# Kernel tuning notes

Hardware: AMD Instinct MI355X
Metric: run time of the kernel (lower is better)

The kernel has to match this reference:

```python
import jax, jax.numpy as jnp
import numpy as np

N_HEAD = 16
EPS = 1e-6


def setup_inputs() -> dict:
    key = jax.random.key(0)
    k1, k2, k3 = jax.random.split(key, 3)
    B, T, C = 2, 2048, 1024
    x = jax.random.normal(k1, (B, T, C), dtype=jnp.float32)
    w_attn = jax.random.normal(k2, (C, 3 * C), dtype=jnp.float32) * 0.02
    w_proj = jax.random.normal(k3, (C, C), dtype=jnp.float32) * 0.02
    return {"x": x, "w_attn": w_attn, "w_proj": w_proj}


def _linear_attention(q, k, v):
    """q,k,v: (T,B,H,D) with q,k already feature-mapped (elu+1).
    Causal linear attention via a D x D running-state recurrence (same math
    as cumsum of k-v outer products, computed without the O(T*D^2) tensor)."""
    B, H, D = q.shape[1], q.shape[2], q.shape[3]

    def step(carry, qkv_t):
        S, z = carry                      # S:(B,H,D,D), z:(B,H,D)
        qt, kt, vt = qkv_t                # each (B,H,D)
        S = S + kt[..., :, None] * vt[..., None, :]
        z = z + kt
        num = jnp.einsum('bhi,bhij->bhj', qt, S)
        den = jnp.sum(qt * z, axis=-1, keepdims=True)
        return (S, z), num / (den + EPS)

    S0 = jnp.zeros((B, H, D, D), q.dtype)
    z0 = jnp.zeros((B, H, D), q.dtype)
    _, y = jax.lax.scan(step, (S0, z0), (q, k, v))
    return y                              # (T,B,H,D)


def reference(x, w_attn, w_proj):
    B, T, C = x.shape
    H = N_HEAD
    D = C // H
    qkv = x @ w_attn                      # (B,T,3C)
    q, k, v = jnp.split(qkv, 3, axis=-1)

    def to_tbhd(a):                       # (B,T,C) -> (T,B,H,D)
        return a.reshape(B, T, H, D).transpose(1, 0, 2, 3)

    q = jax.nn.elu(to_tbhd(q)) + 1.0      # phi(x) = ELU(x)+1
    k = jax.nn.elu(to_tbhd(k)) + 1.0
    v = to_tbhd(v)

    y = _linear_attention(q, k, v)        # (T,B,H,D)
    y = y.transpose(1, 0, 2, 3).reshape(B, T, C)
    return y @ w_proj                     # resid dropout p=0.0 is identity
```

## Files before the change

kernel.cpp:

```cpp
#include <hip/hip_runtime.h>
#include <hip/hip_bf16.h>
#include <cmath>

#define TB   2048
#define CCH  1024
#define NCH  32
#define EPSF 1e-6f

typedef unsigned short u16;
typedef __attribute__((ext_vector_type(8))) short  frag8;
typedef __attribute__((ext_vector_type(4))) float  floatx4;

__device__ __forceinline__ u16 f2bf(float f) {
    unsigned int u = __float_as_uint(f);
    unsigned int r = (u + 0x7fffu + ((u >> 16) & 1u)) >> 16;
    return (u16)r;
}
__device__ __forceinline__ float bf2f(u16 v) {
    return __uint_as_float(((unsigned int)v) << 16);
}

__global__ __launch_bounds__(256) void cvt_bf16_k(
    const float* __restrict__ in, u16* __restrict__ out, int n)
{
    int i = (blockIdx.x * 256 + threadIdx.x) * 8;
    if (i >= n) return;
    float4 a = *(const float4*)(in + i);
    float4 b = *(const float4*)(in + i + 4);
    u16 v[8];
    v[0] = f2bf(a.x); v[1] = f2bf(a.y); v[2] = f2bf(a.z); v[3] = f2bf(a.w);
    v[4] = f2bf(b.x); v[5] = f2bf(b.y); v[6] = f2bf(b.z); v[7] = f2bf(b.w);
    *(uint4*)(out + i) = *(uint4*)v;
}

__global__ __launch_bounds__(256) void transpose_bf16_k(
    const float* __restrict__ in, u16* __restrict__ out, int K, int N)
{
    __shared__ u16 t[64][65];
    const int k0 = blockIdx.y * 64, n0 = blockIdx.x * 64;
    const int c = threadIdx.x & 63, r0 = threadIdx.x >> 6;
    for (int r = r0; r < 64; r += 4)
        t[c][r] = f2bf(in[(size_t)(k0 + r) * N + n0 + c]);
    __syncthreads();
    for (int r = r0; r < 64; r += 4)
        out[(size_t)(n0 + r) * K + k0 + c] = t[r][c];
}

__global__ __launch_bounds__(256) void gemm_bf16_bf16out_k(
    const u16* __restrict__ A, const u16* __restrict__ BT,
    u16* __restrict__ C, int N, int K, int phi_cols)
{
    __shared__ u16 Als[128][72];
    __shared__ u16 Bls[128][72];
    const int tid  = threadIdx.x;
    const int wave = tid >> 6, lane = tid & 63;
    const int quad = lane >> 4, lrow = lane & 15;
    const int wm = wave >> 1, wn = wave & 1;
    const int row0 = blockIdx.y * 128, col0 = blockIdx.x * 128;

    floatx4 acc[4][4] = {};

    for (int k0 = 0; k0 < K; k0 += 64) {
        __syncthreads();
        #pragma unroll
        for (int j = 0; j < 4; ++j) {
            int chunk = tid + 256 * j;
            int r = chunk >> 3, c8 = (chunk & 7) * 8;
            *(uint4*)&Als[r][c8] = *(const uint4*)(A  + (size_t)(row0 + r) * K + k0 + c8);
            *(uint4*)&Bls[r][c8] = *(const uint4*)(BT + (size_t)(col0 + r) * K + k0 + c8);
        }
        __syncthreads();
        #pragma unroll
        for (int ks = 0; ks < 64; ks += 32) {
            frag8 af[4], bf[4];
            #pragma unroll
            for (int i = 0; i < 4; ++i)
                af[i] = *(const frag8*)&Als[wm * 64 + i * 16 + lrow][ks + quad * 8];
            #pragma unroll
            for (int i = 0; i < 4; ++i)
                bf[i] = *(const frag8*)&Bls[wn * 64 + i * 16 + lrow][ks + quad * 8];
            #pragma unroll
            for (int i = 0; i < 4; ++i)
                #pragma unroll
                for (int jn = 0; jn < 4; ++jn)
                    acc[i][jn] = __builtin_amdgcn_mfma_f32_16x16x32_bf16(
                        af[i], bf[jn], acc[i][jn], 0, 0, 0);
        }
    }

    #pragma unroll
    for (int i = 0; i < 4; ++i) {
        #pragma unroll
        for (int jn = 0; jn < 4; ++jn) {
            int col = col0 + wn * 64 + jn * 16 + lrow;
            bool isphi = col < phi_cols;
            #pragma unroll
            for (int r = 0; r < 4; ++r) {
                int row = row0 + wm * 64 + i * 16 + quad * 4 + r;
                float v = acc[i][jn][r];
                if (isphi) v = (v > 0.f) ? (v + 1.f) : __expf(v);
                C[(size_t)row * N + col] = f2bf(v);
            }
        }
    }
}

__global__ __launch_bounds__(256) void gemm_bf16_f32out_k(
    const u16* __restrict__ A, const u16* __restrict__ BT,
    float* __restrict__ C, int N, int K)
{
    __shared__ u16 Als[128][72];
    __shared__ u16 Bls[128][72];
    const int tid  = threadIdx.x;
    const int wave = tid >> 6, lane = tid & 63;
    const int quad = lane >> 4, lrow = lane & 15;
    const int wm = wave >> 1, wn = wave & 1;
    const int row0 = blockIdx.y * 128, col0 = blockIdx.x * 128;

    floatx4 acc[4][4] = {};

    for (int k0 = 0; k0 < K; k0 += 64) {
        __syncthreads();
        #pragma unroll
        for (int j = 0; j < 4; ++j) {
            int chunk = tid + 256 * j;
            int r = chunk >> 3, c8 = (chunk & 7) * 8;
            *(uint4*)&Als[r][c8] = *(const uint4*)(A  + (size_t)(row0 + r) * K + k0 + c8);
            *(uint4*)&Bls[r][c8] = *(const uint4*)(BT + (size_t)(col0 + r) * K + k0 + c8);
        }
        __syncthreads();
        #pragma unroll
        for (int ks = 0; ks < 64; ks += 32) {
            frag8 af[4], bf[4];
            #pragma unroll
            for (int i = 0; i < 4; ++i)
                af[i] = *(const frag8*)&Als[wm * 64 + i * 16 + lrow][ks + quad * 8];
            #pragma unroll
            for (int i = 0; i < 4; ++i)
                bf[i] = *(const frag8*)&Bls[wn * 64 + i * 16 + lrow][ks + quad * 8];
            #pragma unroll
            for (int i = 0; i < 4; ++i)
                #pragma unroll
                for (int jn = 0; jn < 4; ++jn)
                    acc[i][jn] = __builtin_amdgcn_mfma_f32_16x16x32_bf16(
                        af[i], bf[jn], acc[i][jn], 0, 0, 0);
        }
    }

    #pragma unroll
    for (int i = 0; i < 4; ++i)
        #pragma unroll
        for (int jn = 0; jn < 4; ++jn) {
            int col = col0 + wn * 64 + jn * 16 + lrow;
            #pragma unroll
            for (int r = 0; r < 4; ++r) {
                int row = row0 + wm * 64 + i * 16 + quad * 4 + r;
                C[(size_t)row * N + col] = acc[i][jn][r];
            }
        }
}

__global__ __launch_bounds__(256) void chunk_kv_mfma_k(
    const u16* __restrict__ qkv,
    float* __restrict__ Sloc,
    float* __restrict__ zloc)
{
    __shared__ u16 Kt[64][72];
    __shared__ u16 Vt[64][72];
    const int tid  = threadIdx.x;
    const int wave = tid >> 6, lane = tid & 63;
    const int quad = lane >> 4, lrow = lane & 15;
    const int blk = blockIdx.x;
    const int c = blk & 31, h = (blk >> 5) & 15, b = blk >> 9;
    const int t0 = c * 64;
    const u16* base = qkv + (size_t)(b * TB + t0) * 3072 + h * 64;

    #pragma unroll
    for (int m = 0; m < 2; ++m) {
        int chunk = tid + 256 * m;
        int s = chunk >> 3, d0 = (chunk & 7) * 8;
        const u16* row = base + (size_t)s * 3072;
        u16 kv[8], vv[8];
        *(uint4*)kv = *(const uint4*)(row + 1024 + d0);
        *(uint4*)vv = *(const uint4*)(row + 2048 + d0);
        #pragma unroll
        for (int q = 0; q < 8; ++q) { Kt[d0 + q][s] = kv[q]; Vt[d0 + q][s] = vv[q]; }
    }
    __syncthreads();

    frag8 vf[2];
    #pragma unroll
    for (int ks = 0; ks < 2; ++ks)
        vf[ks] = *(const frag8*)&Vt[wave * 16 + lrow][ks * 32 + quad * 8];
    float* So = Sloc + (size_t)blk * 4096;
    #pragma unroll
    for (int jn = 0; jn < 4; ++jn) {
        floatx4 acc = {};
        #pragma unroll
        for (int ks = 0; ks < 2; ++ks) {
            frag8 kf = *(const frag8*)&Kt[jn * 16 + lrow][ks * 32 + quad * 8];
            acc = __builtin_amdgcn_mfma_f32_16x16x32_bf16(vf[ks], kf, acc, 0, 0, 0);
        }
        #pragma unroll
        for (int r = 0; r < 4; ++r) {
            int j = wave * 16 + quad * 4 + r;
            int i = jn * 16 + lrow;
            So[j * 64 + i] = acc[r];
        }
    }
    if (tid < 64) {
        float z = 0.f;
        for (int s = 0; s < 64; ++s) z += bf2f(Kt[tid][s]);
        zloc[(size_t)blk * 64 + tid] = z;
    }
}

__global__ __launch_bounds__(256) void scan_state_k(
    const float* __restrict__ Sloc, u16* __restrict__ Spt, float* __restrict__ z)
{
    const int bh = blockIdx.x >> 4;
    const int part = blockIdx.x & 15;
    const int e0 = part * 256 + threadIdx.x;
    const size_t base = (size_t)bh * NCH * 4096;
    float r = 0.f;
    for (int c = 0; c < NCH; ++c) {
        float t = Sloc[base + (size_t)c * 4096 + e0];
        Spt[base + (size_t)c * 4096 + e0] = f2bf(r);
        r += t;
    }
    if (part == 0 && threadIdx.x < 64) {
        const size_t zb = (size_t)bh * NCH * 64;
        float rz = 0.f;
        for (int c = 0; c < NCH; ++c) {
            float t = z[zb + c * 64 + threadIdx.x];
            z[zb + c * 64 + threadIdx.x] = rz;
            rz += t;
        }
    }
}

__global__ __launch_bounds__(256) void attn_mfma_k(
    const u16* __restrict__ qkv,
    const u16* __restrict__ SptG,
    const float* __restrict__ zp,
    u16* __restrict__ Yb)
{
    __shared__ u16 Qs[64][72];
    __shared__ u16 Ks[64][72];
    __shared__ u16 Vt[64][72];
    __shared__ u16 Sp[64][72];
    __shared__ u16 As[64][72];
    __shared__ float zps[64];
    __shared__ float den4[64][4];
    __shared__ float den[64];

    const int tid  = threadIdx.x;
    const int wave = tid >> 6, lane = tid & 63;
    const int quad = lane >> 4, lrow = lane & 15;
    const int blk = blockIdx.x;
    const int c = blk & 31, h = (blk >> 5) & 15, b = blk >> 9;
    const int t0 = c * 64;
    const u16* base = qkv + (size_t)(b * TB + t0) * 3072 + h * 64;

    #pragma unroll
    for (int m = 0; m < 2; ++m) {
        int chunk = tid + 256 * m;
        int s = chunk >> 3, d0 = (chunk & 7) * 8;
        const u16* row = base + (size_t)s * 3072;
        *(uint4*)&Qs[s][d0] = *(const uint4*)(row + d0);
        *(uint4*)&Ks[s][d0] = *(const uint4*)(row + 1024 + d0);
        u16 vv[8];
        *(uint4*)vv = *(const uint4*)(row + 2048 + d0);
        #pragma unroll
        for (int q = 0; q < 8; ++q) Vt[d0 + q][s] = vv[q];
        *(uint4*)&Sp[s][d0] = *(const uint4*)(SptG + (size_t)blk * 4096 + chunk * 8);
    }
    if (tid < 64) zps[tid] = zp[(size_t)blk * 64 + tid];
    __syncthreads();

    frag8 qf[2];
    #pragma unroll
    for (int ks = 0; ks < 2; ++ks)
        qf[ks] = *(const frag8*)&Qs[wave * 16 + lrow][ks * 32 + quad * 8];

    floatx4 yacc[4] = {}, kacc[4] = {};
    #pragma unroll
    for (int jn = 0; jn < 4; ++jn) {
        #pragma unroll
        for (int ks = 0; ks < 2; ++ks) {
            frag8 spf = *(const frag8*)&Sp[jn * 16 + lrow][ks * 32 + quad * 8];
            yacc[jn] = __builtin_amdgcn_mfma_f32_16x16x32_bf16(qf[ks], spf, yacc[jn], 0, 0, 0);
            frag8 kf = *(const frag8*)&Ks[jn * 16 + lrow][ks * 32 + quad * 8];
            kacc[jn] = __builtin_amdgcn_mfma_f32_16x16x32_bf16(qf[ks], kf, kacc[jn], 0, 0, 0);
        }
    }

    #pragma unroll
    for (int jn = 0; jn < 4; ++jn) {
        int s = jn * 16 + lrow;
        #pragma unroll
        for (int r = 0; r < 4; ++r) {
            int t = wave * 16 + quad * 4 + r;
            float v = (s <= t) ? kacc[jn][r] : 0.f;
            As[t][s] = f2bf(v);
        }
    }
    __syncthreads();

    {
        int t = tid >> 2, seg = tid & 3;
        float p = 0.f;
        #pragma unroll
        for (int i = 0; i < 16; ++i) {
            int d = seg * 16 + i;
            p += bf2f(Qs[t][d]) * zps[d] + bf2f(As[t][d]);
        }
        den4[t][seg] = p;
    }

    frag8 af2[2];
    #pragma unroll
    for (int ks = 0; ks < 2; ++ks)
        af2[ks] = *(const frag8*)&As[wave * 16 + lrow][ks * 32 + quad * 8];
    #pragma unroll
    for (int jn = 0; jn < 4; ++jn)
        #pragma unroll
        for (int ks = 0; ks < 2; ++ks) {
            frag8 vf = *(const frag8*)&Vt[jn * 16 + lrow][ks * 32 + quad * 8];
            yacc[jn] = __builtin_amdgcn_mfma_f32_16x16x32_bf16(af2[ks], vf, yacc[jn], 0, 0, 0);
        }
    __syncthreads();
    if (tid < 64) den[tid] = den4[tid][0] + den4[tid][1] + den4[tid][2] + den4[tid][3];
    __syncthreads();

    #pragma unroll
    for (int jn = 0; jn < 4; ++jn) {
        #pragma unroll
        for (int r = 0; r < 4; ++r) {
            int t = wave * 16 + quad * 4 + r;
            float inv = 1.f / (den[t] + EPSF);
            Qs[t][jn * 16 + lrow] = f2bf(yacc[jn][r] * inv);
        }
    }
    __syncthreads();
    {
        int row = tid >> 2, seg = tid & 3;
        size_t o = (size_t)(b * TB + t0 + row) * CCH + h * 64 + seg * 16;
        *(uint4*)(Yb + o)     = *(uint4*)&Qs[row][seg * 16];
        *(uint4*)(Yb + o + 8) = *(uint4*)&Qs[row][seg * 16 + 8];
    }
}

extern "C" void kernel_launch(void* const* d_in, const int* in_sizes, int n_in,
                              void* d_out, int out_size, void* d_ws, size_t ws_size,
                              hipStream_t stream)
{
    const float* x      = (const float*)d_in[0];
    const float* w_attn = (const float*)d_in[1];
    const float* w_proj = (const float*)d_in[2];
    float* out = (float*)d_out;

    u16* xb    = (u16*)d_ws;
    u16* waT   = xb   + (size_t)4096 * 1024;
    u16* wpT   = waT  + (size_t)3072 * 1024;
    u16* Yb    = wpT  + (size_t)1024 * 1024;
    u16* qkv_b = Yb   + (size_t)4096 * 1024;
    u16* Spt   = qkv_b + (size_t)4096 * 3072;
    float* Sloc = (float*)(Spt + (size_t)1024 * 4096);
    float* zloc = Sloc + (size_t)1024 * 4096;

    cvt_bf16_k      <<<2048, 256, 0, stream>>>(x, xb, 4096 * 1024);
    transpose_bf16_k<<<dim3(48, 16), 256, 0, stream>>>(w_attn, waT, 1024, 3072);
    transpose_bf16_k<<<dim3(16, 16), 256, 0, stream>>>(w_proj, wpT, 1024, 1024);

    gemm_bf16_bf16out_k<<<dim3(24, 32), 256, 0, stream>>>(xb, waT, qkv_b, 3072, 1024, 2048);

    chunk_kv_mfma_k<<<1024, 256, 0, stream>>>(qkv_b, Sloc, zloc);
    scan_state_k   <<<512,  256, 0, stream>>>(Sloc, Spt, zloc);
    attn_mfma_k    <<<1024, 256, 0, stream>>>(qkv_b, Spt, zloc, Yb);

    gemm_bf16_f32out_k<<<dim3(8, 32), 256, 0, stream>>>(Yb, wpT, out, 1024, 1024);
}
```

Baseline: 181.0 us.

## Fuse prep kernels, use async global-to-LDS loads in GEMMs, store chunk states as bf16

Merges the x conversion and the two weight transposes into one prep kernel launch. Both GEMMs now stage tiles with global_load_lds direct-to-LDS 16-byte loads into unpadded shared buffers instead of going through registers. The per-chunk KV state is written as bf16 and scanned in place, which removes the separate fp32 Sloc buffer and halves that traffic. The risks are LDS bank conflicts from dropping the padding, a possibly wrong lane-to-address mapping in the async loads, and some added rounding from storing the local states in bf16.

```diff
diff --git a/kernel.cpp b/kernel.cpp
--- a/kernel.cpp
+++ b/kernel.cpp
@@ -20,24 +20,39 @@
     return __uint_as_float(((unsigned int)v) << 16);
 }
 
-__global__ __launch_bounds__(256) void cvt_bf16_k(
-    const float* __restrict__ in, u16* __restrict__ out, int n)
-{
-    int i = (blockIdx.x * 256 + threadIdx.x) * 8;
-    if (i >= n) return;
-    float4 a = *(const float4*)(in + i);
-    float4 b = *(const float4*)(in + i + 4);
-    u16 v[8];
-    v[0] = f2bf(a.x); v[1] = f2bf(a.y); v[2] = f2bf(a.z); v[3] = f2bf(a.w);
-    v[4] = f2bf(b.x); v[5] = f2bf(b.y); v[6] = f2bf(b.z); v[7] = f2bf(b.w);
-    *(uint4*)(out + i) = *(uint4*)v;
-}
-
-__global__ __launch_bounds__(256) void transpose_bf16_k(
-    const float* __restrict__ in, u16* __restrict__ out, int K, int N)
+__device__ __forceinline__ void async_load16(const u16* g, u16* l) {
+    __builtin_amdgcn_global_load_lds(
+        (const __attribute__((address_space(1))) void*)g,
+        (__attribute__((address_space(3))) void*)l,
+        16, 0, 0);
+}
+
+__global__ __launch_bounds__(256) void prep_k(
+    const float* __restrict__ x, const float* __restrict__ wa,
+    const float* __restrict__ wp,
+    u16* __restrict__ xb, u16* __restrict__ waT, u16* __restrict__ wpT)
 {
     __shared__ u16 t[64][65];
-    const int k0 = blockIdx.y * 64, n0 = blockIdx.x * 64;
+    int blk = blockIdx.x;
+    if (blk < 2048) {
+        int i = (blk * 256 + threadIdx.x) * 8;
+        float4 a = *(const float4*)(x + i);
+        float4 b = *(const float4*)(x + i + 4);
+        u16 v[8];
+        v[0] = f2bf(a.x); v[1] = f2bf(a.y); v[2] = f2bf(a.z); v[3] = f2bf(a.w);
+        v[4] = f2bf(b.x); v[5] = f2bf(b.y); v[6] = f2bf(b.z); v[7] = f2bf(b.w);
+        *(uint4*)(xb + i) = *(uint4*)v;
+        return;
+    }
+    const float* in; u16* out; int K, N, bx, by;
+    if (blk < 2048 + 768) {
+        int tb = blk - 2048; in = wa; out = waT; K = 1024; N = 3072;
+        bx = tb % 48; by = tb / 48;
+    } else {
+        int tb = blk - 2816; in = wp; out = wpT; K = 1024; N = 1024;
+        bx = tb & 15; by = tb >> 4;
+    }
+    const int k0 = by * 64, n0 = bx * 64;
     const int c = threadIdx.x & 63, r0 = threadIdx.x >> 6;
     for (int r = r0; r < 64; r += 4)
         t[c][r] = f2bf(in[(size_t)(k0 + r) * N + n0 + c]);
@@ -50,24 +65,23 @@
     const u16* __restrict__ A, const u16* __restrict__ BT,
     u16* __restrict__ C, int N, int K, int phi_cols)
 {
-    __shared__ u16 Als[128][72];
-    __shared__ u16 Bls[128][72];
+    __shared__ u16 Als[128 * 64];
+    __shared__ u16 Bls[128 * 64];
     const int tid  = threadIdx.x;
     const int wave = tid >> 6, lane = tid & 63;
     const int quad = lane >> 4, lrow = lane & 15;
     const int wm = wave >> 1, wn = wave & 1;
     const int row0 = blockIdx.y * 128, col0 = blockIdx.x * 128;
-
+    const int lr = lane >> 3, lc = (lane & 7) * 8;
     floatx4 acc[4][4] = {};
 
     for (int k0 = 0; k0 < K; k0 += 64) {
         __syncthreads();
         #pragma unroll
-        for (int j = 0; j < 4; ++j) {
-            int chunk = tid + 256 * j;
-            int r = chunk >> 3, c8 = (chunk & 7) * 8;
-            *(uint4*)&Als[r][c8] = *(const uint4*)(A  + (size_t)(row0 + r) * K + k0 + c8);
-            *(uint4*)&Bls[r][c8] = *(const uint4*)(BT + (size_t)(col0 + r) * K + k0 + c8);
+        for (int m = 0; m < 4; ++m) {
+            int i = wave * 4 + m;
+            async_load16(A  + (size_t)(row0 + i * 8 + lr) * K + k0 + lc, &Als[i * 512]);
+            async_load16(BT + (size_t)(col0 + i * 8 + lr) * K + k0 + lc, &Bls[i * 512]);
         }
         __syncthreads();
         #pragma unroll
@@ -75,10 +89,10 @@
             frag8 af[4], bf[4];
             #pragma unroll
             for (int i = 0; i < 4; ++i)
-                af[i] = *(const frag8*)&Als[wm * 64 + i * 16 + lrow][ks + quad * 8];
-            #pragma unroll
-            for (int i = 0; i < 4; ++i)
-                bf[i] = *(const frag8*)&Bls[wn * 64 + i * 16 + lrow][ks + quad * 8];
+                af[i] = *(const frag8*)&Als[(wm * 64 + i * 16 + lrow) * 64 + ks + quad * 8];
+            #pragma unroll
+            for (int i = 0; i < 4; ++i)
+                bf[i] = *(const frag8*)&Bls[(wn * 64 + i * 16 + lrow) * 64 + ks + quad * 8];
             #pragma unroll
             for (int i = 0; i < 4; ++i)
                 #pragma unroll
@@ -109,24 +123,23 @@
     const u16* __restrict__ A, const u16* __restrict__ BT,
     float* __restrict__ C, int N, int K)
 {
-    __shared__ u16 Als[128][72];
-    __shared__ u16 Bls[128][72];
+    __shared__ u16 Als[128 * 64];
+    __shared__ u16 Bls[128 * 64];
     const int tid  = threadIdx.x;
     const int wave = tid >> 6, lane = tid & 63;
     const int quad = lane >> 4, lrow = lane & 15;
     const int wm = wave >> 1, wn = wave & 1;
     const int row0 = blockIdx.y * 128, col0 = blockIdx.x * 128;
-
+    const int lr = lane >> 3, lc = (lane & 7) * 8;
     floatx4 acc[4][4] = {};
 
     for (int k0 = 0; k0 < K; k0 += 64) {
         __syncthreads();
         #pragma unroll
-        for (int j = 0; j < 4; ++j) {
-            int chunk = tid + 256 * j;
-            int r = chunk >> 3, c8 = (chunk & 7) * 8;
-            *(uint4*)&Als[r][c8] = *(const uint4*)(A  + (size_t)(row0 + r) * K + k0 + c8);
-            *(uint4*)&Bls[r][c8] = *(const uint4*)(BT + (size_t)(col0 + r) * K + k0 + c8);
+        for (int m = 0; m < 4; ++m) {
+            int i = wave * 4 + m;
+            async_load16(A  + (size_t)(row0 + i * 8 + lr) * K + k0 + lc, &Als[i * 512]);
+            async_load16(BT + (size_t)(col0 + i * 8 + lr) * K + k0 + lc, &Bls[i * 512]);
         }
         __syncthreads();
         #pragma unroll
@@ -134,10 +147,10 @@
             frag8 af[4], bf[4];
             #pragma unroll
             for (int i = 0; i < 4; ++i)
-                af[i] = *(const frag8*)&Als[wm * 64 + i * 16 + lrow][ks + quad * 8];
-            #pragma unroll
-            for (int i = 0; i < 4; ++i)
-                bf[i] = *(const frag8*)&Bls[wn * 64 + i * 16 + lrow][ks + quad * 8];
+                af[i] = *(const frag8*)&Als[(wm * 64 + i * 16 + lrow) * 64 + ks + quad * 8];
+            #pragma unroll
+            for (int i = 0; i < 4; ++i)
+                bf[i] = *(const frag8*)&Bls[(wn * 64 + i * 16 + lrow) * 64 + ks + quad * 8];
             #pragma unroll
             for (int i = 0; i < 4; ++i)
                 #pragma unroll
@@ -162,7 +175,7 @@
 
 __global__ __launch_bounds__(256) void chunk_kv_mfma_k(
     const u16* __restrict__ qkv,
-    float* __restrict__ Sloc,
+    u16* __restrict__ Spt,
     float* __restrict__ zloc)
 {
     __shared__ u16 Kt[64][72];
@@ -192,7 +205,7 @@
     #pragma unroll
     for (int ks = 0; ks < 2; ++ks)
         vf[ks] = *(const frag8*)&Vt[wave * 16 + lrow][ks * 32 + quad * 8];
-    float* So = Sloc + (size_t)blk * 4096;
+    u16* So = Spt + (size_t)blk * 4096;
     #pragma unroll
     for (int jn = 0; jn < 4; ++jn) {
         floatx4 acc = {};
@@ -205,7 +218,7 @@
         for (int r = 0; r < 4; ++r) {
             int j = wave * 16 + quad * 4 + r;
             int i = jn * 16 + lrow;
-            So[j * 64 + i] = acc[r];
+            So[j * 64 + i] = f2bf(acc[r]);
         }
     }
     if (tid < 64) {
@@ -216,7 +229,7 @@
 }
 
 __global__ __launch_bounds__(256) void scan_state_k(
-    const float* __restrict__ Sloc, u16* __restrict__ Spt, float* __restrict__ z)
+    u16* __restrict__ Spt, float* __restrict__ z)
 {
     const int bh = blockIdx.x >> 4;
     const int part = blockIdx.x & 15;
@@ -224,8 +237,9 @@
     const size_t base = (size_t)bh * NCH * 4096;
     float r = 0.f;
     for (int c = 0; c < NCH; ++c) {
-        float t = Sloc[base + (size_t)c * 4096 + e0];
-        Spt[base + (size_t)c * 4096 + e0] = f2bf(r);
+        u16* p = Spt + base + (size_t)c * 4096 + e0;
+        float t = bf2f(*p);
+        *p = f2bf(r);
         r += t;
     }
     if (part == 0 && threadIdx.x < 64) {
@@ -361,22 +375,19 @@
     float* out = (float*)d_out;
 
     u16* xb    = (u16*)d_ws;
-    u16* waT   = xb   + (size_t)4096 * 1024;
-    u16* wpT   = waT  + (size_t)3072 * 1024;
-    u16* Yb    = wpT  + (size_t)1024 * 1024;
-    u16* qkv_b = Yb   + (size_t)4096 * 1024;
+    u16* waT   = xb    + (size_t)4096 * 1024;
+    u16* wpT   = waT   + (size_t)3072 * 1024;
+    u16* Yb    = wpT   + (size_t)1024 * 1024;
+    u16* qkv_b = Yb    + (size_t)4096 * 1024;
     u16* Spt   = qkv_b + (size_t)4096 * 3072;
-    float* Sloc = (float*)(Spt + (size_t)1024 * 4096);
-    float* zloc = Sloc + (size_t)1024 * 4096;
-
-    cvt_bf16_k      <<<2048, 256, 0, stream>>>(x, xb, 4096 * 1024);
-    transpose_bf16_k<<<dim3(48, 16), 256, 0, stream>>>(w_attn, waT, 1024, 3072);
-    transpose_bf16_k<<<dim3(16, 16), 256, 0, stream>>>(w_proj, wpT, 1024, 1024);
+    float* zloc = (float*)(Spt + (size_t)1024 * 4096);
+
+    prep_k<<<3072, 256, 0, stream>>>(x, w_attn, w_proj, xb, waT, wpT);
 
     gemm_bf16_bf16out_k<<<dim3(24, 32), 256, 0, stream>>>(xb, waT, qkv_b, 3072, 1024, 2048);
 
-    chunk_kv_mfma_k<<<1024, 256, 0, stream>>>(qkv_b, Sloc, zloc);
-    scan_state_k   <<<512,  256, 0, stream>>>(Sloc, Spt, zloc);
+    chunk_kv_mfma_k<<<1024, 256, 0, stream>>>(qkv_b, Spt, zloc);
+    scan_state_k   <<<512,  256, 0, stream>>>(Spt, zloc);
     attn_mfma_k    <<<1024, 256, 0, stream>>>(qkv_b, Spt, zloc, Yb);
 
     gemm_bf16_f32out_k<<<dim3(8, 32), 256, 0, stream>>>(Yb, wpT, out, 1024, 1024);
```

Result: no change. 181.6 us (+0.3%).
